# Optimization experiments

Hardware: AMD Instinct MI355X
Metric: run time of the kernel (lower is better)

The kernel has to match this reference:

```python
import jax, jax.numpy as jnp
import numpy as np

NUM_HEADS = 12
DIM_HEAD = 64
HIDDEN = 768


def _get_rel_pos(size, rel_pos):
    # q_size == k_size: relative coords in [0, 2*size-2]
    idx = jnp.arange(size)[:, None] - jnp.arange(size)[None, :] + (size - 1)
    return rel_pos[idx]  # (size, size, dim_head)


def setup_inputs() -> dict:
    key = jax.random.key(0)
    ks = jax.random.split(key, 5)
    B, H, W, C = 4, 32, 32, HIDDEN
    x = jax.random.normal(ks[0], (B, H, W, C), dtype=jnp.float32)
    w_qkv = jax.random.normal(ks[1], (C, 3 * NUM_HEADS * DIM_HEAD), dtype=jnp.float32) * (C ** -0.5)
    w_out = jax.random.normal(ks[2], (NUM_HEADS * DIM_HEAD, C), dtype=jnp.float32) * ((NUM_HEADS * DIM_HEAD) ** -0.5)
    b_out = jnp.zeros((C,), dtype=jnp.float32)
    rel_pos_h = jax.random.normal(ks[3], (2 * H - 1, DIM_HEAD), dtype=jnp.float32) * 0.02
    rel_pos_w = jax.random.normal(ks[4], (2 * W - 1, DIM_HEAD), dtype=jnp.float32) * 0.02
    return {"x": x, "w_qkv": w_qkv, "w_out": w_out, "b_out": b_out,
            "rel_pos_h": rel_pos_h, "rel_pos_w": rel_pos_w}


def reference(x, w_qkv, w_out, b_out, rel_pos_h, rel_pos_w):
    B, H, W, C = x.shape
    N = H * W
    nh, dh = NUM_HEADS, DIM_HEAD
    # qkv projection: (B, N, 3*nh*dh) split as (qkv, head, dim)
    qkv = x.reshape(B, N, C) @ w_qkv
    qkv = qkv.reshape(B, N, 3, nh, dh).transpose(2, 0, 3, 1, 4)  # (3, B, nh, N, dh)
    q, k, v = qkv[0], qkv[1], qkv[2]
    scale = dh ** -0.5
    attn = jnp.einsum('bhnd,bhmd->bhnm', q, k) * scale  # (B, nh, N, N)
    # decomposed relative positional bias (heads folded into batch)
    Rh = _get_rel_pos(H, rel_pos_h)  # (H, H, dh)
    Rw = _get_rel_pos(W, rel_pos_w)  # (W, W, dh)
    r_q = q.reshape(B * nh, H, W, dh)
    rel_h = jnp.einsum('bhwc,hkc->bhwk', r_q, Rh)  # (B*nh, H, W, H)
    rel_w = jnp.einsum('bhwc,wkc->bhwk', r_q, Rw)  # (B*nh, H, W, W)
    attn = (attn.reshape(B * nh, H, W, H, W)
            + rel_h[:, :, :, :, None]
            + rel_w[:, :, :, None, :]).reshape(B, nh, N, N)
    attn = jax.nn.softmax(attn, axis=-1)
    out = jnp.einsum('bhnm,bhmd->bhnd', attn, v)  # (B, nh, N, dh)
    out = out.transpose(0, 2, 1, 3).reshape(B, N, nh * dh)
    return out @ w_out + b_out  # (B, N, hidden)
```

## Files before the change

### kernel.cpp

```cpp
#include <hip/hip_runtime.h>
#include <cstdint>

#define DEV __device__ __forceinline__

typedef __bf16  bf16x8 __attribute__((ext_vector_type(8)));
typedef short   s16x8  __attribute__((ext_vector_type(8)));
typedef float   f32x4  __attribute__((ext_vector_type(4)));

#define QSCALE 0.18033688011112042f
#define MOFF   17.312340490667560f

DEV unsigned short f2bf(float f){
  union { float f; unsigned u; } v; v.f = f;
  unsigned r = v.u + 0x7fffu + ((v.u >> 16) & 1u);
  return (unsigned short)(r >> 16);
}

DEV unsigned pk2(float lo, float hi){
  unsigned a = __builtin_bit_cast(unsigned, lo) + 0x8000u;
  unsigned b = __builtin_bit_cast(unsigned, hi) + 0x8000u;
  return __builtin_amdgcn_perm(b, a, 0x07060302);
}

DEV void gl2lds16(const void* g, void* l){
  __builtin_amdgcn_global_load_lds((__attribute__((address_space(1))) void*)(void*)(g),
                                   (__attribute__((address_space(3))) void*)(l), 16, 0, 0);
}

DEV f32x4 mfma16(bf16x8 a, bf16x8 b, f32x4 c){
  return __builtin_amdgcn_mfma_f32_16x16x32_bf16(a, b, c, 0, 0, 0);
}

__global__ __launch_bounds__(256) void prep_kernel(const float* __restrict__ x,
                                                   short* __restrict__ xb,
                                                   const float* __restrict__ rph,
                                                   const float* __restrict__ rpw,
                                                   short* __restrict__ rphb,
                                                   short* __restrict__ rpwb,
                                                   const float* __restrict__ w_qkv,
                                                   short* __restrict__ wqT,
                                                   const float* __restrict__ w_out,
                                                   short* __restrict__ woT){
  __shared__ float tb[32][33];
  int b = blockIdx.x;
  if (b < 1536){
    int i = b * 256 + threadIdx.x;
    const float4* in4 = (const float4*)x;
    float4 f0 = in4[i*2], f1 = in4[i*2+1];
    s16x8 o;
    o[0]=(short)f2bf(f0.x); o[1]=(short)f2bf(f0.y); o[2]=(short)f2bf(f0.z); o[3]=(short)f2bf(f0.w);
    o[4]=(short)f2bf(f1.x); o[5]=(short)f2bf(f1.y); o[6]=(short)f2bf(f1.z); o[7]=(short)f2bf(f1.w);
    *(s16x8*)(xb + i*8) = o;
  } else if (b == 1536){
    int t = threadIdx.x;
    for (int j = 0; j < 16; j++){
      int idx = t*16 + j;
      if (idx < 4032){
        rphb[idx] = (short)f2bf(rph[idx] * 8.f);
        rpwb[idx] = (short)f2bf(rpw[idx] * 8.f);
      } else if (idx < 4096){
        rpwb[idx] = 0;
      }
    }
  } else {
    const float* in; short* out; int R, C, bx, by;
    if (b < 3265){ int t = b - 1537; in = w_qkv; out = wqT; R = 768; C = 2304; bx = t % 72; by = t / 72; }
    else         { int t = b - 3265; in = w_out; out = woT; R = 768; C = 768;  bx = t % 24; by = t / 24; }
    int tx = threadIdx.x & 31, ty = threadIdx.x >> 5;
    int c0 = bx * 32, r0 = by * 32;
    for (int i = 0; i < 4; i++)
      tb[ty + i*8][tx] = in[(r0 + ty + i*8)*C + c0 + tx];
    __syncthreads();
    for (int i = 0; i < 4; i++)
      out[(c0 + ty + i*8)*R + r0 + tx] = (short)f2bf(tb[tx][ty + i*8]);
  }
}

__global__ __launch_bounds__(256) void qkv_gemm_kernel(const short* __restrict__ xb,
                                                       const short* __restrict__ wqT,
                                                       short* __restrict__ qb,
                                                       short* __restrict__ kb,
                                                       short* __restrict__ vtb){
  __shared__ __align__(16) short As[128*64];
  __shared__ __align__(16) short Bs[96*64];
  const int tid = threadIdx.x, lane = tid & 63, wv = tid >> 6;
  const int quad = lane >> 4, mi = lane & 15;
  const int flat = blockIdx.x + (blockIdx.y << 5);
  const int xcd = flat & 7, s = flat >> 3;
  const int bx = (xcd & 3)*8 + (s & 7);
  const int by = (xcd >> 2)*12 + (s >> 3);
  const int m0 = bx * 128, n0 = by * 96;
  const int wrow = wv >> 1, wcol = wv & 1;
  const int srow = lane >> 3;
  const int sc = (lane & 7) ^ (srow & 7);
  f32x4 acc[4][3] = {};
  for (int k0 = 0; k0 < 768; k0 += 64){
    __syncthreads();
    for (int i = 0; i < 4; i++){
      int rbase = i*32 + wv*8;
      int row = rbase + srow;
      gl2lds16(xb + (m0+row)*768 + k0 + sc*8, As + rbase*64 + lane*8);
    }
    for (int i = 0; i < 3; i++){
      int rbase = i*32 + wv*8;
      int row = rbase + srow;
      gl2lds16(wqT + (n0+row)*768 + k0 + sc*8, Bs + rbase*64 + lane*8);
    }
    __syncthreads();
    bf16x8 a[2][4], b[2][3];
#pragma unroll
    for (int kk = 0; kk < 2; kk++){
      int ccs = ((quad + kk*4) ^ (mi & 7)) * 8;
      for (int mt = 0; mt < 4; mt++) a[kk][mt] = *(const bf16x8*)(As + (wrow*64 + mt*16 + mi)*64 + ccs);
      for (int nt = 0; nt < 3; nt++) b[kk][nt] = *(const bf16x8*)(Bs + (wcol*48 + nt*16 + mi)*64 + ccs);
    }
#pragma unroll
    for (int kk = 0; kk < 2; kk++)
      for (int mt = 0; mt < 4; mt++)
        for (int nt = 0; nt < 3; nt++)
          acc[mt][nt] = mfma16(a[kk][mt], b[kk][nt], acc[mt][nt]);
  }
  const int which = n0 / 768;
  if (which == 2){
    for (int nt = 0; nt < 3; nt++){
      int j = n0 + wcol*48 + nt*16 + mi;
      int rem = j % 768;
      int head = rem >> 6, d = rem & 63;
      for (int mt = 0; mt < 4; mt++)
        for (int r = 0; r < 4; r++){
          int m = m0 + wrow*64 + mt*16 + quad*4 + r;
          int bh = (m >> 10)*12 + head;
          vtb[((bh*64 + d) << 10) + (m & 1023)] = (short)f2bf(acc[mt][nt][r]);
        }
    }
  } else {
    const float qs = (which == 0) ? QSCALE : 1.0f;
    short* dst = (which == 0) ? qb : kb;
    for (int nt = 0; nt < 3; nt++){
      int j = n0 + wcol*48 + nt*16 + mi;
      int rem = j % 768;
      int head = rem >> 6, d = rem & 63;
      for (int mt = 0; mt < 4; mt++)
        for (int r = 0; r < 4; r++){
          int m = m0 + wrow*64 + mt*16 + quad*4 + r;
          int bh = (m >> 10)*12 + head;
          dst[((bh << 10) + (m & 1023))*64 + d] = (short)f2bf(acc[mt][nt][r] * qs);
        }
    }
  }
}

__global__ __launch_bounds__(256, 4) void flash_kernel(const short* __restrict__ qb,
                                                       const short* __restrict__ kb,
                                                       const short* __restrict__ vtb,
                                                       const short* __restrict__ rphb,
                                                       const short* __restrict__ rpwb,
                                                       short* __restrict__ ao){
  __shared__ __align__(16) char smem[32768];
  float* Es  = (float*)smem;
  short* Kt  = (short*)smem;
  short* Vt  = (short*)(smem + 8192);
  short* Qt  = (short*)(smem + 16384);
  short* Pt  = (short*)(smem + 16384);
  float* rHs = (float*)(smem + 24576);
  const int tid = threadIdx.x, lane = tid & 63, wv = tid >> 6;
  const int quad = lane >> 4, mi = lane & 15;
  const int flat = blockIdx.x + (blockIdx.y << 4);
  const int nw = (flat & 7)*96 + (flat >> 3);
  const int bh = nw >> 4, n0 = (nw & 15) << 6;
  const int sw0 = (quad ^ (mi & 7)) * 8;
  const int sw1 = ((quad + 4) ^ (mi & 7)) * 8;
  const int qrow = wv*16 + mi;
  const int srow = lane >> 3;

  const short* kg = kb  + bh*1024*64;
  const short* vg = vtb + bh*64*1024;

  {
    const short* qg = qb + (bh*1024 + n0)*64;
#pragma unroll
    for (int i = 0; i < 2; i++){
      int slab = wv*2 + i, rbase = slab*8;
      int row = rbase + srow;
      int c = (lane & 7) ^ (row & 7);
      gl2lds16(qg + row*64 + c*8, Qt + rbase*64 + lane*8);
    }
  }
  __syncthreads();

  bf16x8 qf0 = *(const bf16x8*)(Qt + qrow*64 + sw0);
  bf16x8 qf1 = *(const bf16x8*)(Qt + qrow*64 + sw1);

  {
    int h = (n0 + wv*16) >> 5;
    const short* rp = rphb + (h + 31 - mi)*64;
#pragma unroll
    for (int khb = 0; khb < 2; khb++){
      const short* rk = rp - khb*1024;
      bf16x8 a0 = *(const bf16x8*)(rk + quad*8);
      bf16x8 a1 = *(const bf16x8*)(rk + 32 + quad*8);
      f32x4 c = {};
      c = mfma16(a0, qf0, c);
      c = mfma16(a1, qf1, c);
      for (int r = 0; r < 4; r++)
        rHs[(khb*16 + quad*4 + r)*64 + wv*16 + mi] = c[r] - MOFF;
    }
  }

#pragma unroll
  for (int jt = 0; jt < 4; jt++){
    const short* rr = rpwb + (jt*16 + mi)*64;
    bf16x8 a0 = *(const bf16x8*)(rr + quad*8);
    bf16x8 a1 = *(const bf16x8*)(rr + 32 + quad*8);
    f32x4 c = {};
    c = mfma16(a0, qf0, c);
    c = mfma16(a1, qf1, c);
    for (int r = 0; r < 4; r++)
      Es[(jt*16 + quad*4 + r)*64 + qrow] = c[r];
  }
  float rw[2][4];
  {
    int w31 = (qrow & 31) + 31;
#pragma unroll
    for (int s = 0; s < 2; s++)
      for (int r = 0; r < 4; r++)
        rw[s][r] = Es[(w31 - (s*16 + quad*4 + r))*64 + qrow];
  }

  __syncthreads();

  f32x4 O[4] = {};
  float l_ = 0.f;

#pragma unroll 1
  for (int step = 0; step < 16; step++){
    {
      const short* kt = kg + step*4096;
#pragma unroll
      for (int i = 0; i < 2; i++){
        int slab = wv*2 + i, rbase = slab*8;
        int row = rbase + srow;
        int c = (lane & 7) ^ (row & 7);
        gl2lds16(kt + row*64 + c*8, Kt + rbase*64 + lane*8);
        gl2lds16(vg + row*1024 + step*64 + c*8, Vt + rbase*64 + lane*8);
      }
    }
    __syncthreads();

    f32x4 S[4];
#pragma unroll
    for (int nt = 0; nt < 4; nt++){
      bf16x8 kf0 = *(const bf16x8*)(Kt + (nt*16 + mi)*64 + sw0);
      bf16x8 kf1 = *(const bf16x8*)(Kt + (nt*16 + mi)*64 + sw1);
      f32x4 c = {};
      c = mfma16(kf0, qf0, c);
      c = mfma16(kf1, qf1, c);
      S[nt] = c;
    }
    float kh0 = rHs[(2*step)*64 + qrow];
    float kh1 = rHs[(2*step + 1)*64 + qrow];
#pragma unroll
    for (int nt = 0; nt < 4; nt++){
      float kh = (nt & 2) ? kh1 : kh0;
      for (int r = 0; r < 4; r++){
        float p = __builtin_amdgcn_exp2f(S[nt][r] + kh + rw[nt & 1][r]);
        S[nt][r] = p;
        l_ += p;
      }
    }
#pragma unroll
    for (int nt = 0; nt < 4; nt++){
      unsigned u0 = pk2(S[nt][0], S[nt][1]);
      unsigned u1 = pk2(S[nt][2], S[nt][3]);
      int chunk = (2*nt + (quad >> 1)) ^ (mi & 7);
      uint2 uu; uu.x = u0; uu.y = u1;
      *(uint2*)(Pt + qrow*64 + chunk*8 + (quad & 1)*4) = uu;
    }
    bf16x8 p0 = *(const bf16x8*)(Pt + qrow*64 + sw0);
    bf16x8 p1 = *(const bf16x8*)(Pt + qrow*64 + sw1);
#pragma unroll
    for (int t = 0; t < 4; t++){
      bf16x8 v0 = *(const bf16x8*)(Vt + (t*16 + mi)*64 + sw0);
      bf16x8 v1 = *(const bf16x8*)(Vt + (t*16 + mi)*64 + sw1);
      O[t] = mfma16(p0, v0, O[t]);
      O[t] = mfma16(p1, v1, O[t]);
    }
    __syncthreads();
  }

  l_ += __shfl_xor(l_, 16, 64);
  l_ += __shfl_xor(l_, 32, 64);
  float inv[4];
#pragma unroll
  for (int r = 0; r < 4; r++) inv[r] = 1.f / __shfl(l_, quad*4 + r, 64);
  int b_ = bh / 12, head = bh % 12;
#pragma unroll
  for (int t = 0; t < 4; t++)
    for (int r = 0; r < 4; r++){
      int n = n0 + wv*16 + quad*4 + r;
      ao[(b_*1024 + n)*768 + head*64 + t*16 + mi] = (short)f2bf(O[t][r] * inv[r]);
    }
}

__global__ __launch_bounds__(256) void proj_kernel(const short* __restrict__ ao,
                                                   const short* __restrict__ woT,
                                                   const float* __restrict__ bias,
                                                   float* __restrict__ out){
  __shared__ __align__(16) short As[64*64];
  __shared__ __align__(16) short Bs[96*64];
  const int tid = threadIdx.x, lane = tid & 63, wv = tid >> 6;
  const int quad = lane >> 4, mi = lane & 15;
  const int m0 = blockIdx.x * 64, n0 = blockIdx.y * 96;
  const int wrow = wv >> 1, wcol = wv & 1;
  const int srow = lane >> 3, sc = (lane & 7) ^ (srow & 7);
  f32x4 acc[2][3] = {};
  for (int k0 = 0; k0 < 768; k0 += 64){
    __syncthreads();
    for (int i = 0; i < 2; i++){
      int rbase = i*32 + wv*8, row = rbase + srow;
      gl2lds16(ao + (m0+row)*768 + k0 + sc*8, As + rbase*64 + lane*8);
    }
    for (int i = 0; i < 3; i++){
      int rbase = i*32 + wv*8, row = rbase + srow;
      gl2lds16(woT + (n0+row)*768 + k0 + sc*8, Bs + rbase*64 + lane*8);
    }
    __syncthreads();
    bf16x8 a[2][2], b[2][3];
#pragma unroll
    for (int kk = 0; kk < 2; kk++){
      int ccs = ((quad + kk*4) ^ (mi & 7)) * 8;
      for (int mt = 0; mt < 2; mt++) a[kk][mt] = *(const bf16x8*)(As + (wrow*32 + mt*16 + mi)*64 + ccs);
      for (int nt = 0; nt < 3; nt++) b[kk][nt] = *(const bf16x8*)(Bs + (wcol*48 + nt*16 + mi)*64 + ccs);
    }
#pragma unroll
    for (int kk = 0; kk < 2; kk++)
      for (int mt = 0; mt < 2; mt++)
        for (int nt = 0; nt < 3; nt++)
          acc[mt][nt] = mfma16(a[kk][mt], b[kk][nt], acc[mt][nt]);
  }
  for (int nt = 0; nt < 3; nt++){
    int j = n0 + wcol*48 + nt*16 + mi;
    float bj = bias[j];
    for (int mt = 0; mt < 2; mt++)
      for (int r = 0; r < 4; r++){
        int m = m0 + wrow*32 + mt*16 + quad*4 + r;
        out[m*768 + j] = acc[mt][nt][r] + bj;
      }
  }
}

extern "C" void kernel_launch(void* const* d_in, const int* in_sizes, int n_in,
                              void* d_out, int out_size, void* d_ws, size_t ws_size,
                              hipStream_t stream){
  const float* x     = (const float*)d_in[0];
  const float* w_qkv = (const float*)d_in[1];
  const float* w_out = (const float*)d_in[2];
  const float* b_out = (const float*)d_in[3];
  const float* rph   = (const float*)d_in[4];
  const float* rpw   = (const float*)d_in[5];
  float* out = (float*)d_out;
  char* ws = (char*)d_ws;
  short* xb    = (short*)(ws + 0);
  short* wqT   = (short*)(ws + 6291456);
  short* woT   = (short*)(ws + 9830400);
  short* qb    = (short*)(ws + 11010048);
  short* kb    = (short*)(ws + 17301504);
  short* vtb   = (short*)(ws + 29884416);
  short* rphb  = (short*)(ws + 48758784);
  short* rpwb  = (short*)(ws + 48775168);
  short* ao    = xb;

  prep_kernel<<<3841, 256, 0, stream>>>(x, xb, rph, rpw, rphb, rpwb, w_qkv, wqT, w_out, woT);
  qkv_gemm_kernel<<<dim3(32, 24), 256, 0, stream>>>(xb, wqT, qb, kb, vtb);
  flash_kernel<<<dim3(16, 48), 256, 0, stream>>>(qb, kb, vtb, rphb, rpwb, ao);
  proj_kernel<<<dim3(64, 8), 256, 0, stream>>>(ao, woT, b_out, out);
}
```

Measured before the change: 152.7 us.

## Process 128 query rows per flash block to reuse each K/V tile twice

Each flash-attention workgroup now handles 128 query rows instead of 64, with every wave computing two 16-row query fragments against the same K/V tile in LDS. This halves the K/V global loads and LDS staging per query and gives more MFMA work per barrier. In exchange it doubles register use per thread (two accumulator sets), enlarges shared memory to 48 KB, lowers the occupancy target to 2, and halves the grid to 384 blocks, which may underfill the 256 CUs.

New measurement: 158.0 us. 3.5% more time.

```diff
diff --git a/kernel.cpp b/kernel.cpp
--- a/kernel.cpp
+++ b/kernel.cpp
@@ -150,37 +150,38 @@
   }
 }
 
-__global__ __launch_bounds__(256, 4) void flash_kernel(const short* __restrict__ qb,
+__global__ __launch_bounds__(256, 2) void flash_kernel(const short* __restrict__ qb,
                                                        const short* __restrict__ kb,
                                                        const short* __restrict__ vtb,
                                                        const short* __restrict__ rphb,
                                                        const short* __restrict__ rpwb,
                                                        short* __restrict__ ao){
-  __shared__ __align__(16) char smem[32768];
-  float* Es  = (float*)smem;
+  __shared__ __align__(16) char smem[49152];
+  short* Qt  = (short*)smem;
   short* Kt  = (short*)smem;
   short* Vt  = (short*)(smem + 8192);
-  short* Qt  = (short*)(smem + 16384);
+  float* Es  = (float*)smem;
   short* Pt  = (short*)(smem + 16384);
-  float* rHs = (float*)(smem + 24576);
+  float* rHs = (float*)(smem + 32768);
   const int tid = threadIdx.x, lane = tid & 63, wv = tid >> 6;
   const int quad = lane >> 4, mi = lane & 15;
-  const int flat = blockIdx.x + (blockIdx.y << 4);
-  const int nw = (flat & 7)*96 + (flat >> 3);
-  const int bh = nw >> 4, n0 = (nw & 15) << 6;
+  const int srow = lane >> 3;
+  const int flat = blockIdx.x + (blockIdx.y << 3);
+  const int nw = (flat & 7)*48 + (flat >> 3);
+  const int bh = nw >> 3, n0 = (nw & 7) << 7;
   const int sw0 = (quad ^ (mi & 7)) * 8;
   const int sw1 = ((quad + 4) ^ (mi & 7)) * 8;
-  const int qrow = wv*16 + mi;
-  const int srow = lane >> 3;
-
-  const short* kg = kb  + bh*1024*64;
-  const short* vg = vtb + bh*64*1024;
+  const int qa = wv*16 + mi;
+  const int qbr = 64 + qa;
+
+  const short* kg = kb  + bh*65536;
+  const short* vg = vtb + bh*65536;
 
   {
-    const short* qg = qb + (bh*1024 + n0)*64;
-#pragma unroll
-    for (int i = 0; i < 2; i++){
-      int slab = wv*2 + i, rbase = slab*8;
+    const short* qg = qb + ((bh << 10) + n0)*64;
+#pragma unroll
+    for (int i = 0; i < 4; i++){
+      int slab = wv*4 + i, rbase = slab*8;
       int row = rbase + srow;
       int c = (lane & 7) ^ (row & 7);
       gl2lds16(qg + row*64 + c*8, Qt + rbase*64 + lane*8);
@@ -188,49 +189,72 @@
   }
   __syncthreads();
 
-  bf16x8 qf0 = *(const bf16x8*)(Qt + qrow*64 + sw0);
-  bf16x8 qf1 = *(const bf16x8*)(Qt + qrow*64 + sw1);
+  bf16x8 qA0 = *(const bf16x8*)(Qt + qa*64 + sw0);
+  bf16x8 qA1 = *(const bf16x8*)(Qt + qa*64 + sw1);
+  bf16x8 qB0 = *(const bf16x8*)(Qt + qbr*64 + sw0);
+  bf16x8 qB1 = *(const bf16x8*)(Qt + qbr*64 + sw1);
 
   {
-    int h = (n0 + wv*16) >> 5;
-    const short* rp = rphb + (h + 31 - mi)*64;
+    int ha = (n0 + wv*16) >> 5;
+    int hb = (n0 + 64 + wv*16) >> 5;
+    const short* rpA = rphb + (ha + 31 - mi)*64;
+    const short* rpB = rphb + (hb + 31 - mi)*64;
 #pragma unroll
     for (int khb = 0; khb < 2; khb++){
-      const short* rk = rp - khb*1024;
-      bf16x8 a0 = *(const bf16x8*)(rk + quad*8);
-      bf16x8 a1 = *(const bf16x8*)(rk + 32 + quad*8);
-      f32x4 c = {};
-      c = mfma16(a0, qf0, c);
-      c = mfma16(a1, qf1, c);
-      for (int r = 0; r < 4; r++)
-        rHs[(khb*16 + quad*4 + r)*64 + wv*16 + mi] = c[r] - MOFF;
-    }
-  }
+      {
+        const short* rk = rpA - khb*1024;
+        bf16x8 a0 = *(const bf16x8*)(rk + quad*8);
+        bf16x8 a1 = *(const bf16x8*)(rk + 32 + quad*8);
+        f32x4 c = {};
+        c = mfma16(a0, qA0, c);
+        c = mfma16(a1, qA1, c);
+        for (int r = 0; r < 4; r++)
+          rHs[(khb*16 + quad*4 + r)*128 + qa] = c[r] - MOFF;
+      }
+      {
+        const short* rk = rpB - khb*1024;
+        bf16x8 a0 = *(const bf16x8*)(rk + quad*8);
+        bf16x8 a1 = *(const bf16x8*)(rk + 32 + quad*8);
+        f32x4 c = {};
+        c = mfma16(a0, qB0, c);
+        c = mfma16(a1, qB1, c);
+        for (int r = 0; r < 4; r++)
+          rHs[(khb*16 + quad*4 + r)*128 + qbr] = c[r] - MOFF;
+      }
+    }
+  }
+
+  __syncthreads();
 
 #pragma unroll
   for (int jt = 0; jt < 4; jt++){
     const short* rr = rpwb + (jt*16 + mi)*64;
     bf16x8 a0 = *(const bf16x8*)(rr + quad*8);
     bf16x8 a1 = *(const bf16x8*)(rr + 32 + quad*8);
-    f32x4 c = {};
-    c = mfma16(a0, qf0, c);
-    c = mfma16(a1, qf1, c);
-    for (int r = 0; r < 4; r++)
-      Es[(jt*16 + quad*4 + r)*64 + qrow] = c[r];
-  }
-  float rw[2][4];
+    f32x4 cA = {}, cB = {};
+    cA = mfma16(a0, qA0, cA); cA = mfma16(a1, qA1, cA);
+    cB = mfma16(a0, qB0, cB); cB = mfma16(a1, qB1, cB);
+    for (int r = 0; r < 4; r++){
+      Es[(jt*16 + quad*4 + r)*128 + qa]  = cA[r];
+      Es[(jt*16 + quad*4 + r)*128 + qbr] = cB[r];
+    }
+  }
+  float rwA[2][4], rwB[2][4];
   {
-    int w31 = (qrow & 31) + 31;
+    int w31 = (qa & 31) + 31;
 #pragma unroll
     for (int s = 0; s < 2; s++)
-      for (int r = 0; r < 4; r++)
-        rw[s][r] = Es[(w31 - (s*16 + quad*4 + r))*64 + qrow];
+      for (int r = 0; r < 4; r++){
+        int row = w31 - (s*16 + quad*4 + r);
+        rwA[s][r] = Es[row*128 + qa];
+        rwB[s][r] = Es[row*128 + qbr];
+      }
   }
 
   __syncthreads();
 
-  f32x4 O[4] = {};
-  float l_ = 0.f;
+  f32x4 OA[4] = {}, OB[4] = {};
+  float lA = 0.f, lB = 0.f;
 
 #pragma unroll 1
   for (int step = 0; step < 16; step++){
@@ -247,58 +271,67 @@
     }
     __syncthreads();
 
-    f32x4 S[4];
+    f32x4 SA[4], SB[4];
 #pragma unroll
     for (int nt = 0; nt < 4; nt++){
       bf16x8 kf0 = *(const bf16x8*)(Kt + (nt*16 + mi)*64 + sw0);
       bf16x8 kf1 = *(const bf16x8*)(Kt + (nt*16 + mi)*64 + sw1);
-      f32x4 c = {};
-      c = mfma16(kf0, qf0, c);
-      c = mfma16(kf1, qf1, c);
-      S[nt] = c;
-    }
-    float kh0 = rHs[(2*step)*64 + qrow];
-    float kh1 = rHs[(2*step + 1)*64 + qrow];
+      f32x4 cA = {}; cA = mfma16(kf0, qA0, cA); cA = mfma16(kf1, qA1, cA);
+      SA[nt] = cA;
+      f32x4 cB = {}; cB = mfma16(kf0, qB0, cB); cB = mfma16(kf1, qB1, cB);
+      SB[nt] = cB;
+    }
+    float khA0 = rHs[(2*step)*128 + qa],  khA1 = rHs[(2*step + 1)*128 + qa];
+    float khB0 = rHs[(2*step)*128 + qbr], khB1 = rHs[(2*step + 1)*128 + qbr];
 #pragma unroll
     for (int nt = 0; nt < 4; nt++){
-      float kh = (nt & 2) ? kh1 : kh0;
+      float khA = (nt & 2) ? khA1 : khA0;
+      float khB = (nt & 2) ? khB1 : khB0;
       for (int r = 0; r < 4; r++){
-        float p = __builtin_amdgcn_exp2f(S[nt][r] + kh + rw[nt & 1][r]);
-        S[nt][r] = p;
-        l_ += p;
+        float pA = __builtin_amdgcn_exp2f(SA[nt][r] + khA + rwA[nt & 1][r]);
+        SA[nt][r] = pA; lA += pA;
+        float pB = __builtin_amdgcn_exp2f(SB[nt][r] + khB + rwB[nt & 1][r]);
+        SB[nt][r] = pB; lB += pB;
       }
     }
 #pragma unroll
     for (int nt = 0; nt < 4; nt++){
-      unsigned u0 = pk2(S[nt][0], S[nt][1]);
-      unsigned u1 = pk2(S[nt][2], S[nt][3]);
       int chunk = (2*nt + (quad >> 1)) ^ (mi & 7);
-      uint2 uu; uu.x = u0; uu.y = u1;
-      *(uint2*)(Pt + qrow*64 + chunk*8 + (quad & 1)*4) = uu;
-    }
-    bf16x8 p0 = *(const bf16x8*)(Pt + qrow*64 + sw0);
-    bf16x8 p1 = *(const bf16x8*)(Pt + qrow*64 + sw1);
+      uint2 uA; uA.x = pk2(SA[nt][0], SA[nt][1]); uA.y = pk2(SA[nt][2], SA[nt][3]);
+      *(uint2*)(Pt + qa*64 + chunk*8 + (quad & 1)*4) = uA;
+      uint2 uB; uB.x = pk2(SB[nt][0], SB[nt][1]); uB.y = pk2(SB[nt][2], SB[nt][3]);
+      *(uint2*)(Pt + qbr*64 + chunk*8 + (quad & 1)*4) = uB;
+    }
+    bf16x8 pa0 = *(const bf16x8*)(Pt + qa*64 + sw0);
+    bf16x8 pa1 = *(const bf16x8*)(Pt + qa*64 + sw1);
+    bf16x8 pb0 = *(const bf16x8*)(Pt + qbr*64 + sw0);
+    bf16x8 pb1 = *(const bf16x8*)(Pt + qbr*64 + sw1);
 #pragma unroll
     for (int t = 0; t < 4; t++){
       bf16x8 v0 = *(const bf16x8*)(Vt + (t*16 + mi)*64 + sw0);
       bf16x8 v1 = *(const bf16x8*)(Vt + (t*16 + mi)*64 + sw1);
-      O[t] = mfma16(p0, v0, O[t]);
-      O[t] = mfma16(p1, v1, O[t]);
-    }
-    __syncthreads();
-  }
-
-  l_ += __shfl_xor(l_, 16, 64);
-  l_ += __shfl_xor(l_, 32, 64);
-  float inv[4];
-#pragma unroll
-  for (int r = 0; r < 4; r++) inv[r] = 1.f / __shfl(l_, quad*4 + r, 64);
+      OA[t] = mfma16(pa0, v0, OA[t]); OA[t] = mfma16(pa1, v1, OA[t]);
+      OB[t] = mfma16(pb0, v0, OB[t]); OB[t] = mfma16(pb1, v1, OB[t]);
+    }
+    __syncthreads();
+  }
+
+  lA += __shfl_xor(lA, 16, 64); lA += __shfl_xor(lA, 32, 64);
+  lB += __shfl_xor(lB, 16, 64); lB += __shfl_xor(lB, 32, 64);
+  float invA[4], invB[4];
+#pragma unroll
+  for (int r = 0; r < 4; r++){
+    invA[r] = 1.f / __shfl(lA, quad*4 + r, 64);
+    invB[r] = 1.f / __shfl(lB, quad*4 + r, 64);
+  }
   int b_ = bh / 12, head = bh % 12;
 #pragma unroll
   for (int t = 0; t < 4; t++)
     for (int r = 0; r < 4; r++){
-      int n = n0 + wv*16 + quad*4 + r;
-      ao[(b_*1024 + n)*768 + head*64 + t*16 + mi] = (short)f2bf(O[t][r] * inv[r]);
+      int nA = n0 + wv*16 + quad*4 + r;
+      int nB = nA + 64;
+      ao[(b_*1024 + nA)*768 + head*64 + t*16 + mi] = (short)f2bf(OA[t][r] * invA[r]);
+      ao[(b_*1024 + nB)*768 + head*64 + t*16 + mi] = (short)f2bf(OB[t][r] * invB[r]);
     }
 }
 
@@ -372,6 +405,6 @@
 
   prep_kernel<<<3841, 256, 0, stream>>>(x, xb, rph, rpw, rphb, rpwb, w_qkv, wqT, w_out, woT);
   qkv_gemm_kernel<<<dim3(32, 24), 256, 0, stream>>>(xb, wqT, qb, kb, vtb);
-  flash_kernel<<<dim3(16, 48), 256, 0, stream>>>(qb, kb, vtb, rphb, rpwb, ao);
+  flash_kernel<<<dim3(8, 48), 256, 0, stream>>>(qb, kb, vtb, rphb, rpwb, ao);
   proj_kernel<<<dim3(64, 8), 256, 0, stream>>>(ao, woT, b_out, out);
 }
```
